# Performance work log

Measured on AMD Instinct MI355X. Metric: run time of the kernel, lower is better.

## Reference

```python
import jax, jax.numpy as jnp
import numpy as np
from jax import lax

N = 8192
TARGET_COMPONENTS = 1.0
TARGET_CYCLES = 0.0
WEIGHT = 1.0
THRESH_SHIFT = 2.0


def setup_inputs() -> dict:
    key = jax.random.key(0)
    x = jax.random.normal(key, (N, N), dtype=jnp.float32)
    # symmetrize so directed DFS traversal == undirected connectivity,
    # then shift so adj > 0 is sparse (realistic learned graph structure)
    adj = (x + x.T) * 0.5 - THRESH_SHIFT
    return {"adj": adj}


def _count_components(adj):
    """Connected components via min-label propagation (parallel equivalent
    of the serial DFS in the torch module for a symmetric adjacency)."""
    n = adj.shape[0]
    pos = adj > 0  # [n, n] bool edge mask
    labels0 = jnp.arange(n, dtype=jnp.int32)

    def body(state):
        labels, _ = state
        # min label among neighbors (n = sentinel for non-edges)
        neigh_min = jnp.min(jnp.where(pos, labels[None, :], jnp.int32(n)), axis=1)
        new_labels = jnp.minimum(labels, neigh_min)
        return new_labels, jnp.any(new_labels != labels)

    labels, _ = lax.while_loop(lambda s: s[1], body,
                               (labels0, jnp.array(True)))
    # exactly one node per component keeps its own (minimal) index
    return jnp.sum((labels == labels0).astype(jnp.int32))


def reference(adj):
    n = adj.shape[0]
    n_comp = _count_components(adj).astype(jnp.float32)
    n_edges = (jnp.sum((adj > 0).astype(jnp.int32)) // 2).astype(jnp.float32)
    betti_1 = n_edges - jnp.float32(n) + n_comp           # Betti-1 estimate
    n_cycles = jnp.maximum(jnp.float32(0.0), betti_1)
    component_loss = (n_comp - TARGET_COMPONENTS) ** 2
    cycle_loss = (n_cycles - TARGET_CYCLES) ** 2
    return WEIGHT * (component_loss + cycle_loss)
```

## Files before the change

kernel.cpp:

```cpp
#include <hip/hip_runtime.h>


#define NN 8192
#define SCAN_LDS_CAP 2048
#define LBL_THREADS 1024
#define EPT 80
#define REGCAP (LBL_THREADS * EPT)

__global__ __launch_bounds__(64) void init_kernel(int* counters) {
    if (threadIdx.x < 2) counters[threadIdx.x] = 0;
}

__global__ __launch_bounds__(256) void scan_kernel(const float* __restrict__ adj,
                                                   int* __restrict__ counters,
                                                   unsigned int* __restrict__ ebuf,
                                                   int cap) {
    __shared__ int lds_n;
    __shared__ int lds_base;
    __shared__ unsigned int lds_e[SCAN_LDS_CAP];
    if (threadIdx.x == 0) lds_n = 0;
    __syncthreads();

    int b = blockIdx.x;
    int ra = b;
    int rb = NN - 1 - b;
    int nfa = (ra + 4) >> 2;
    int nfb = (rb + 4) >> 2;
    int tot = nfa + nfb;

    int t = threadIdx.x;
    int c1 = 0;

    float4 v[9];
    int   rr[9];
    int   gg[9];
    bool  ok[9];

    #pragma unroll
    for (int k = 0; k < 9; ++k) {
        int vg = t + (k << 8);
        ok[k] = vg < tot;
        bool inA = vg < nfa;
        int r = inA ? ra : rb;
        int g = inA ? vg : vg - nfa;
        rr[k] = r;
        gg[k] = g;
        if (ok[k]) v[k] = ((const float4*)(adj + (size_t)r * NN))[g];
    }

    #pragma unroll
    for (int k = 0; k < 9; ++k) {
        if (!ok[k]) continue;
        int r  = rr[k];
        int j0 = gg[k] << 2;
        float vv[4] = {v[k].x, v[k].y, v[k].z, v[k].w};
        #pragma unroll
        for (int c = 0; c < 4; ++c) {
            int j = j0 + c;
            bool pos = vv[c] > 0.0f;
            if (pos && j < r) {
                int kk = atomicAdd(&lds_n, 1);
                unsigned int e = ((unsigned)r << 13) | (unsigned)j;
                if (kk < SCAN_LDS_CAP) lds_e[kk] = e;
                else {
                    int gk = atomicAdd(counters, 1);
                    if (gk < cap) ebuf[gk] = e;
                }
            }
            c1 += (pos && j == r) ? 1 : 0;
        }
    }

    #pragma unroll
    for (int off = 32; off > 0; off >>= 1) c1 += __shfl_down(c1, off, 64);
    if ((t & 63) == 0 && c1) atomicAdd(counters + 1, c1);

    __syncthreads();
    int n = lds_n < SCAN_LDS_CAP ? lds_n : SCAN_LDS_CAP;
    if (t == 0) lds_base = atomicAdd(counters, n);
    __syncthreads();
    int base = lds_base;
    for (int k = t; k < n; k += 256) {
        int idx = base + k;
        if (idx < cap) ebuf[idx] = lds_e[k];
    }
}

__global__ __launch_bounds__(LBL_THREADS) void label_final_kernel(
        const unsigned int* __restrict__ ebuf,
        const int* __restrict__ counters,
        int cap, float* __restrict__ out) {
    __shared__ int lab[NN];
    __shared__ int changed;
    __shared__ int wsum[LBL_THREADS / 64];
    int tid = threadIdx.x;
    for (int i = tid; i < NN; i += LBL_THREADS) lab[i] = i;

    int total_lower = counters[0];
    int m = total_lower < cap ? total_lower : cap;

    unsigned int e[EPT];
    #pragma unroll
    for (int q = 0; q < EPT; ++q) {
        int idx = tid + q * LBL_THREADS;
        e[q] = (idx < m) ? ebuf[idx] : 0u;
    }
    __syncthreads();

    for (;;) {
        if (tid == 0) changed = 0;
        __syncthreads();

        #pragma unroll
        for (int q = 0; q < EPT; ++q) {
            int r = (int)(e[q] >> 13);
            int j = (int)(e[q] & (NN - 1));
            int lr = lab[r];
            int lj = lab[j];
            if (lj < lr) {
                if (atomicMin(&lab[r], lj) > lj) changed = 1;
            } else if (lr < lj) {
                if (atomicMin(&lab[j], lr) > lr) changed = 1;
            }
        }
        for (int idx = REGCAP + tid; idx < m; idx += LBL_THREADS) {
            unsigned int eg = ebuf[idx];
            int r = (int)(eg >> 13);
            int j = (int)(eg & (NN - 1));
            int lr = lab[r];
            int lj = lab[j];
            if (lj < lr) {
                if (atomicMin(&lab[r], lj) > lj) changed = 1;
            } else if (lr < lj) {
                if (atomicMin(&lab[j], lr) > lr) changed = 1;
            }
        }
        __syncthreads();

        #pragma unroll
        for (int s = 0; s < 3; ++s) {
            for (int i = tid; i < NN; i += LBL_THREADS) {
                int l = lab[i];
                int ll = lab[l];
                if (ll < l) { lab[i] = ll; changed = 1; }
            }
        }
        __syncthreads();

        if (changed == 0) break;
        __syncthreads();
    }

    int cnt = 0;
    for (int i = tid; i < NN; i += LBL_THREADS) cnt += (lab[i] == i) ? 1 : 0;
    #pragma unroll
    for (int off = 32; off > 0; off >>= 1) cnt += __shfl_down(cnt, off, 64);
    if ((tid & 63) == 0) wsum[tid >> 6] = cnt;
    __syncthreads();
    if (tid == 0) {
        int roots = 0;
        #pragma unroll
        for (int w = 0; w < LBL_THREADS / 64; ++w) roots += wsum[w];
        long long total = 2LL * (long long)total_lower + (long long)counters[1];
        long long n_edges_i = total >> 1;
        double n_comp = (double)roots;
        double comp_loss = (n_comp - 1.0) * (n_comp - 1.0);
        double betti = (double)n_edges_i - (double)NN + n_comp;
        double cyc = betti > 0.0 ? betti : 0.0;
        out[0] = (float)(comp_loss + cyc * cyc);
    }
}

extern "C" void kernel_launch(void* const* d_in, const int* in_sizes, int n_in,
                              void* d_out, int out_size, void* d_ws, size_t ws_size,
                              hipStream_t stream) {
    const float* adj = (const float*)d_in[0];
    int* ws = (int*)d_ws;
    int* counters = ws;
    unsigned int* ebuf = (unsigned int*)(ws + 2);
    long long cap_ll = (long long)(ws_size / 4) - 2;
    int cap = cap_ll > 0x7fffffff ? 0x7fffffff : (cap_ll < 0 ? 0 : (int)cap_ll);
    float* out = (float*)d_out;

    init_kernel<<<1, 64, 0, stream>>>(counters);
    scan_kernel<<<NN / 2, 256, 0, stream>>>(adj, counters, ebuf, cap);
    label_final_kernel<<<1, LBL_THREADS, 0, stream>>>(ebuf, counters, cap, out);
}
```

Measured before the change: 431.2 us.

## Group edges by row and give each thread a contiguous edge range in label propagation

```diff
diff --git a/kernel.cpp b/kernel.cpp
--- a/kernel.cpp
+++ b/kernel.cpp
@@ -2,10 +2,8 @@
 
 
 #define NN 8192
-#define SCAN_LDS_CAP 2048
+#define ROW_LDS_CAP 1024
 #define LBL_THREADS 1024
-#define EPT 80
-#define REGCAP (LBL_THREADS * EPT)
 
 __global__ __launch_bounds__(64) void init_kernel(int* counters) {
     if (threadIdx.x < 2) counters[threadIdx.x] = 0;
@@ -15,10 +13,11 @@
                                                    int* __restrict__ counters,
                                                    unsigned int* __restrict__ ebuf,
                                                    int cap) {
-    __shared__ int lds_n;
+    __shared__ int na, nb;
     __shared__ int lds_base;
-    __shared__ unsigned int lds_e[SCAN_LDS_CAP];
-    if (threadIdx.x == 0) lds_n = 0;
+    __shared__ unsigned int ea[ROW_LDS_CAP];
+    __shared__ unsigned int eb[ROW_LDS_CAP];
+    if (threadIdx.x == 0) { na = 0; nb = 0; }
     __syncthreads();
 
     int b = blockIdx.x;
@@ -53,15 +52,16 @@
         if (!ok[k]) continue;
         int r  = rr[k];
         int j0 = gg[k] << 2;
+        bool isA = (r == ra);
         float vv[4] = {v[k].x, v[k].y, v[k].z, v[k].w};
         #pragma unroll
         for (int c = 0; c < 4; ++c) {
             int j = j0 + c;
             bool pos = vv[c] > 0.0f;
             if (pos && j < r) {
-                int kk = atomicAdd(&lds_n, 1);
                 unsigned int e = ((unsigned)r << 13) | (unsigned)j;
-                if (kk < SCAN_LDS_CAP) lds_e[kk] = e;
+                int kk = isA ? atomicAdd(&na, 1) : atomicAdd(&nb, 1);
+                if (kk < ROW_LDS_CAP) { (isA ? ea : eb)[kk] = e; }
                 else {
                     int gk = atomicAdd(counters, 1);
                     if (gk < cap) ebuf[gk] = e;
@@ -76,13 +76,18 @@
     if ((t & 63) == 0 && c1) atomicAdd(counters + 1, c1);
 
     __syncthreads();
-    int n = lds_n < SCAN_LDS_CAP ? lds_n : SCAN_LDS_CAP;
-    if (t == 0) lds_base = atomicAdd(counters, n);
+    int na_c = na < ROW_LDS_CAP ? na : ROW_LDS_CAP;
+    int nb_c = nb < ROW_LDS_CAP ? nb : ROW_LDS_CAP;
+    if (t == 0) lds_base = atomicAdd(counters, na_c + nb_c);
     __syncthreads();
     int base = lds_base;
-    for (int k = t; k < n; k += 256) {
+    for (int k = t; k < na_c; k += 256) {
         int idx = base + k;
-        if (idx < cap) ebuf[idx] = lds_e[k];
+        if (idx < cap) ebuf[idx] = ea[k];
+    }
+    for (int k = t; k < nb_c; k += 256) {
+        int idx = base + na_c + k;
+        if (idx < cap) ebuf[idx] = eb[k];
     }
 }
 
@@ -98,47 +103,49 @@
 
     int total_lower = counters[0];
     int m = total_lower < cap ? total_lower : cap;
-
-    unsigned int e[EPT];
-    #pragma unroll
-    for (int q = 0; q < EPT; ++q) {
-        int idx = tid + q * LBL_THREADS;
-        e[q] = (idx < m) ? ebuf[idx] : 0u;
-    }
-    __syncthreads();
+    int cchunk = (m + LBL_THREADS - 1) / LBL_THREADS;
+    int s = tid * cchunk;
+    int epos = s + cchunk; if (epos > m) epos = m;
+    if (s > m) s = m;
 
     for (;;) {
         if (tid == 0) changed = 0;
         __syncthreads();
 
-        #pragma unroll
-        for (int q = 0; q < EPT; ++q) {
-            int r = (int)(e[q] >> 13);
-            int j = (int)(e[q] & (NN - 1));
-            int lr = lab[r];
-            int lj = lab[j];
-            if (lj < lr) {
-                if (atomicMin(&lab[r], lj) > lj) changed = 1;
-            } else if (lr < lj) {
-                if (atomicMin(&lab[j], lr) > lr) changed = 1;
+        {
+            int cur_r = -1, lr = 0, mu = 0;
+            auto proc = [&](unsigned int eg) {
+                int r = (int)(eg >> 13);
+                int j = (int)(eg & (NN - 1));
+                int lj = lab[j];
+                if (r != cur_r) {
+                    if (cur_r >= 0 && mu < lr) {
+                        if (atomicMin(&lab[cur_r], mu) > mu) changed = 1;
+                    }
+                    cur_r = r; lr = lab[r]; mu = lr;
+                }
+                if (lj < mu) mu = lj;
+                else if (mu < lj) {
+                    if (atomicMin(&lab[j], mu) > mu) changed = 1;
+                }
+            };
+            int idx = s;
+            for (; idx + 4 <= epos; idx += 4) {
+                unsigned int e0 = ebuf[idx];
+                unsigned int e1 = ebuf[idx + 1];
+                unsigned int e2 = ebuf[idx + 2];
+                unsigned int e3 = ebuf[idx + 3];
+                proc(e0); proc(e1); proc(e2); proc(e3);
             }
-        }
-        for (int idx = REGCAP + tid; idx < m; idx += LBL_THREADS) {
-            unsigned int eg = ebuf[idx];
-            int r = (int)(eg >> 13);
-            int j = (int)(eg & (NN - 1));
-            int lr = lab[r];
-            int lj = lab[j];
-            if (lj < lr) {
-                if (atomicMin(&lab[r], lj) > lj) changed = 1;
-            } else if (lr < lj) {
-                if (atomicMin(&lab[j], lr) > lr) changed = 1;
+            for (; idx < epos; ++idx) proc(ebuf[idx]);
+            if (cur_r >= 0 && mu < lr) {
+                if (atomicMin(&lab[cur_r], mu) > mu) changed = 1;
             }
         }
         __syncthreads();
 
         #pragma unroll
-        for (int s = 0; s < 3; ++s) {
+        for (int sc = 0; sc < 2; ++sc) {
             for (int i = tid; i < NN; i += LBL_THREADS) {
                 int l = lab[i];
                 int ll = lab[l];
```

Result: faster. 390.9 us, median of 2 (-9.3%).
